# Kernel tuning notes

Measured on AMD Instinct MI355X. Metric: run time of the kernel, lower is better.

The kernel has to match this reference:

```python
import jax, jax.numpy as jnp
import numpy as np

B, S, H, F, V, MAX_OOV = 128, 512, 1024, 512, 50000, 50


def setup_inputs() -> dict:
    key = jax.random.key(0)
    ks = jax.random.split(key, 20)
    r = lambda i, shp, s=0.02: (jax.random.normal(ks[i], shp, jnp.float32) * s)
    return dict(
        input=jax.random.randint(ks[0], (B,), 0, V),
        hidden=jax.random.normal(ks[1], (1, B, H), jnp.float32) * 0.1,
        encoder_outputs=jax.random.normal(ks[2], (B, S, H), jnp.float32) * 0.1,
        x_padding_masks=jnp.ones((B, S), jnp.float32),
        len_oov=jax.random.randint(ks[3], (B,), 0, MAX_OOV),
        coverage_vector=jnp.zeros((B, S), jnp.float32),
        ref2tgt=jax.random.randint(ks[4], (B, S), 0, V + MAX_OOV),
        emb=r(5, (V, F)),
        W_ih=r(6, (3 * H, F)), W_hh=r(7, (3 * H, H)),
        b_ih=jnp.zeros(3 * H, jnp.float32), b_hh=jnp.zeros(3 * H, jnp.float32),
        e2v1_w=r(8, (F, H)), e2v1_b=jnp.zeros(F, jnp.float32),
        e2v2_w=r(9, (V, F)), e2v2_b=jnp.zeros(V, jnp.float32),
        fc_w=r(10, (H, 2 * H)), fc_b=jnp.zeros(H, jnp.float32),
        wgen_w=r(11, (1, 2 * H + F)), wgen_b=jnp.zeros(1, jnp.float32),
        att_Wh=r(12, (H, H)), att_Ws=r(13, (H, H)),
        att_wc=r(14, (H,)), att_b=jnp.zeros(H, jnp.float32), att_v=r(15, (H,)),
    )


def reference(input, hidden, encoder_outputs, x_padding_masks, len_oov,
              coverage_vector, ref2tgt, emb, W_ih, W_hh, b_ih, b_hh,
              e2v1_w, e2v1_b, e2v2_w, e2v2_b, fc_w, fc_b, wgen_w, wgen_b,
              att_Wh, att_Ws, att_wc, att_b, att_v):
    # embedding lookup (dropout is identity at inference)
    emb_x = emb[input]  # [B, F]

    # --- additive (Bahdanau) attention with coverage ---
    s = hidden[0]  # [B, H] (n_layers == 1)
    feat = jnp.tanh(
        jnp.einsum('bsh,kh->bsk', encoder_outputs, att_Wh)
        + (s @ att_Ws.T)[:, None, :]
        + coverage_vector[:, :, None] * att_wc
        + att_b)  # [B, S, H]
    e = jnp.einsum('bsh,h->bs', feat, att_v)  # [B, S]
    a = jax.nn.softmax(e, axis=1) * x_padding_masks
    a = a / (jnp.sum(a, axis=1, keepdims=True))  # [B, S] renormalized attn
    coverage_new = coverage_vector + a
    context = jnp.einsum('bs,bsh->bh', a, encoder_outputs)  # [B, H]
    h_att = jnp.concatenate([s, context], axis=-1) @ fc_w.T + fc_b  # [B, H]

    # --- single-step GRU (PyTorch gate order r, z, n) ---
    gi = emb_x @ W_ih.T + b_ih  # [B, 3H]
    gh = h_att @ W_hh.T + b_hh  # [B, 3H]
    i_r, i_z, i_n = jnp.split(gi, 3, axis=-1)
    h_r, h_z, h_n = jnp.split(gh, 3, axis=-1)
    r = jax.nn.sigmoid(i_r + h_r)
    z = jax.nn.sigmoid(i_z + h_z)
    n = jnp.tanh(i_n + r * h_n)
    h_new = (1.0 - z) * n + z * h_att  # [B, H]

    # --- vocab distribution ---
    out1 = h_new @ e2v1_w.T + e2v1_b  # [B, F]
    p_vocab = jax.nn.softmax(out1 @ e2v2_w.T + e2v2_b, axis=1)  # [B, V]

    # --- pointer-generator mixing ---
    x_gen = jnp.concatenate([context, h_new, emb_x], axis=-1)  # [B, 2H+F]
    p_gen = jax.nn.sigmoid(x_gen @ wgen_w.T + wgen_b)[:, 0]  # [B]
    p_gen = jnp.clip(p_gen, 0.001, 0.999)
    p_vocab_w = p_gen[:, None] * p_vocab  # [B, V]
    attn_w = (1.0 - p_gen)[:, None] * a  # [B, S]
    p_ext = jnp.concatenate([p_vocab_w, jnp.zeros((B, MAX_OOV), p_vocab_w.dtype)], axis=1)
    rows = jnp.arange(B)[:, None]
    final = p_ext.at[rows, ref2tgt].add(attn_w)  # scatter_add over extended vocab

    return final, h_new[None], coverage_new, a
```

## Files before the change

kernel.cpp:

```cpp
#include <hip/hip_runtime.h>
#include <math.h>

#define B_   128
#define S_   512
#define H_   1024
#define F_   512
#define V_   50000
#define OOV_ 50
#define EV_  (V_ + OOV_)

#define BM 128
#define BN 128
#define BK 64

typedef __attribute__((ext_vector_type(8))) __bf16 bf16x8;
typedef __attribute__((ext_vector_type(4))) __bf16 bf16x4;
typedef __attribute__((ext_vector_type(4))) float  f32x4;

__device__ __forceinline__ void gload_lds16(const void* g, void* lds) {
  __builtin_amdgcn_global_load_lds(
      (const __attribute__((address_space(1))) unsigned int*)g,
      (__attribute__((address_space(3))) unsigned int*)lds, 16, 0, 0);
}

__device__ __forceinline__ float fast_tanh(float x) {
  float v = fminf(fmaxf(x, -15.f), 15.f);
  float t = __expf(2.f * v);
  return 1.f - 2.f / (t + 1.f);
}

__global__ __launch_bounds__(256)
void cast_both_kernel(const float* __restrict__ enc, __bf16* __restrict__ enc_h,
                      const float* __restrict__ wh, __bf16* __restrict__ wh_h)
{
  const size_t n_enc = (size_t)B_ * S_ * H_;
  const size_t n_tot = n_enc + (size_t)H_ * H_;
  for (size_t i = ((size_t)blockIdx.x * 256 + threadIdx.x) * 8; i < n_tot;
       i += (size_t)gridDim.x * 256 * 8) {
    const float* in; __bf16* out; size_t j;
    if (i < n_enc) { in = enc; out = enc_h; j = i; }
    else           { in = wh;  out = wh_h;  j = i - n_enc; }
    float4 a = *(const float4*)(in + j);
    float4 b = *(const float4*)(in + j + 4);
    bf16x8 o;
    o[0] = (__bf16)a.x; o[1] = (__bf16)a.y; o[2] = (__bf16)a.z; o[3] = (__bf16)a.w;
    o[4] = (__bf16)b.x; o[5] = (__bf16)b.y; o[6] = (__bf16)b.z; o[7] = (__bf16)b.w;
    *(bf16x8*)(out + j) = o;
  }
}

__global__ __launch_bounds__(256)
void gemm_splitk(const float* __restrict__ A, const float* __restrict__ W,
                 float* __restrict__ partial, int N, int K, int KS)
{
  __shared__ float As[128 * 68];
  __shared__ float Ws[32 * 68];
  const int tid = threadIdx.x;
  const int n0 = blockIdx.x * 32;
  const int p  = blockIdx.y;
  const int tx = tid & 7, ty = tid >> 3;
  const int lr = tid >> 4, lc4 = (tid & 15) * 4;
  float acc[4][4] = {};
  const int kend = p * KS + KS;
  for (int k0 = p * KS; k0 < kend; k0 += 64) {
#pragma unroll
    for (int pp = 0; pp < 8; ++pp)
      *(float4*)(As + (pp * 16 + lr) * 68 + lc4) =
          *(const float4*)(A + (size_t)(pp * 16 + lr) * K + k0 + lc4);
#pragma unroll
    for (int pp = 0; pp < 2; ++pp)
      *(float4*)(Ws + (pp * 16 + lr) * 68 + lc4) =
          *(const float4*)(W + (size_t)(n0 + pp * 16 + lr) * K + k0 + lc4);
    __syncthreads();
#pragma unroll
    for (int kk = 0; kk < 16; ++kk) {
      float4 av[4], wv[4];
#pragma unroll
      for (int i = 0; i < 4; i++) av[i] = *(const float4*)(As + (ty * 4 + i) * 68 + kk * 4);
#pragma unroll
      for (int j = 0; j < 4; j++) wv[j] = *(const float4*)(Ws + (tx * 4 + j) * 68 + kk * 4);
#pragma unroll
      for (int i = 0; i < 4; i++)
#pragma unroll
        for (int j = 0; j < 4; j++) {
          acc[i][j] = fmaf(av[i].x, wv[j].x, acc[i][j]);
          acc[i][j] = fmaf(av[i].y, wv[j].y, acc[i][j]);
          acc[i][j] = fmaf(av[i].z, wv[j].z, acc[i][j]);
          acc[i][j] = fmaf(av[i].w, wv[j].w, acc[i][j]);
        }
    }
    __syncthreads();
  }
#pragma unroll
  for (int i = 0; i < 4; i++)
#pragma unroll
    for (int j = 0; j < 4; j++)
      partial[((size_t)p * 128 + ty * 4 + i) * N + n0 + tx * 4 + j] = acc[i][j];
}

__global__ __launch_bounds__(256)
void gemm_splitk_cat(const float* __restrict__ A1, const float* __restrict__ A2,
                     const float* __restrict__ W, float* __restrict__ partial,
                     int N, int K, int KS)
{
  __shared__ float As[128 * 68];
  __shared__ float Ws[32 * 68];
  const int tid = threadIdx.x;
  const int n0 = blockIdx.x * 32;
  const int p  = blockIdx.y;
  const int tx = tid & 7, ty = tid >> 3;
  const int lr = tid >> 4, lc4 = (tid & 15) * 4;
  const float* A = (p * KS < 1024) ? A1 : A2;
  const int kbase = (p * KS < 1024) ? 0 : 1024;
  float acc[4][4] = {};
  const int kend = p * KS + KS;
  for (int k0 = p * KS; k0 < kend; k0 += 64) {
#pragma unroll
    for (int pp = 0; pp < 8; ++pp)
      *(float4*)(As + (pp * 16 + lr) * 68 + lc4) =
          *(const float4*)(A + (size_t)(pp * 16 + lr) * 1024 + (k0 - kbase) + lc4);
#pragma unroll
    for (int pp = 0; pp < 2; ++pp)
      *(float4*)(Ws + (pp * 16 + lr) * 68 + lc4) =
          *(const float4*)(W + (size_t)(n0 + pp * 16 + lr) * K + k0 + lc4);
    __syncthreads();
#pragma unroll
    for (int kk = 0; kk < 16; ++kk) {
      float4 av[4], wv[4];
#pragma unroll
      for (int i = 0; i < 4; i++) av[i] = *(const float4*)(As + (ty * 4 + i) * 68 + kk * 4);
#pragma unroll
      for (int j = 0; j < 4; j++) wv[j] = *(const float4*)(Ws + (tx * 4 + j) * 68 + kk * 4);
#pragma unroll
      for (int i = 0; i < 4; i++)
#pragma unroll
        for (int j = 0; j < 4; j++) {
          acc[i][j] = fmaf(av[i].x, wv[j].x, acc[i][j]);
          acc[i][j] = fmaf(av[i].y, wv[j].y, acc[i][j]);
          acc[i][j] = fmaf(av[i].z, wv[j].z, acc[i][j]);
          acc[i][j] = fmaf(av[i].w, wv[j].w, acc[i][j]);
        }
    }
    __syncthreads();
  }
#pragma unroll
  for (int i = 0; i < 4; i++)
#pragma unroll
    for (int j = 0; j < 4; j++)
      partial[((size_t)p * 128 + ty * 4 + i) * N + n0 + tx * 4 + j] = acc[i][j];
}

__global__ __launch_bounds__(256)
void gemm_splitk_gather(const int* __restrict__ input, const float* __restrict__ emb,
                        const float* __restrict__ W, float* __restrict__ partial,
                        int N, int K, int KS)
{
  __shared__ float As[128 * 68];
  __shared__ float Ws[32 * 68];
  const int tid = threadIdx.x;
  const int n0 = blockIdx.x * 32;
  const int p  = blockIdx.y;
  const int tx = tid & 7, ty = tid >> 3;
  const int lr = tid >> 4, lc4 = (tid & 15) * 4;
  float acc[4][4] = {};
  const int kend = p * KS + KS;
  for (int k0 = p * KS; k0 < kend; k0 += 64) {
#pragma unroll
    for (int pp = 0; pp < 8; ++pp) {
      int row = input[pp * 16 + lr];
      *(float4*)(As + (pp * 16 + lr) * 68 + lc4) =
          *(const float4*)(emb + (size_t)row * K + k0 + lc4);
    }
#pragma unroll
    for (int pp = 0; pp < 2; ++pp)
      *(float4*)(Ws + (pp * 16 + lr) * 68 + lc4) =
          *(const float4*)(W + (size_t)(n0 + pp * 16 + lr) * K + k0 + lc4);
    __syncthreads();
#pragma unroll
    for (int kk = 0; kk < 16; ++kk) {
      float4 av[4], wv[4];
#pragma unroll
      for (int i = 0; i < 4; i++) av[i] = *(const float4*)(As + (ty * 4 + i) * 68 + kk * 4);
#pragma unroll
      for (int j = 0; j < 4; j++) wv[j] = *(const float4*)(Ws + (tx * 4 + j) * 68 + kk * 4);
#pragma unroll
      for (int i = 0; i < 4; i++)
#pragma unroll
        for (int j = 0; j < 4; j++) {
          acc[i][j] = fmaf(av[i].x, wv[j].x, acc[i][j]);
          acc[i][j] = fmaf(av[i].y, wv[j].y, acc[i][j]);
          acc[i][j] = fmaf(av[i].z, wv[j].z, acc[i][j]);
          acc[i][j] = fmaf(av[i].w, wv[j].w, acc[i][j]);
        }
    }
    __syncthreads();
  }
#pragma unroll
  for (int i = 0; i < 4; i++)
#pragma unroll
    for (int j = 0; j < 4; j++)
      partial[((size_t)p * 128 + ty * 4 + i) * N + n0 + tx * 4 + j] = acc[i][j];
}

__global__ __launch_bounds__(256)
void reduce_partial(const float* __restrict__ partial, const float* __restrict__ bias,
                    float* __restrict__ C, int N, int P)
{
  int idx = blockIdx.x * 256 + threadIdx.x;
  int n = idx % N;
  float s = bias ? bias[n] : 0.f;
  for (int p = 0; p < P; ++p) s += partial[(size_t)p * 128 * N + idx];
  C[idx] = s;
}

__global__ __launch_bounds__(256)
void reduce_partial_bf16(const float* __restrict__ partial, const float* __restrict__ bias,
                         __bf16* __restrict__ C, int N, int P)
{
  int idx = blockIdx.x * 256 + threadIdx.x;
  int n = idx % N;
  float s = bias ? bias[n] : 0.f;
  for (int p = 0; p < P; ++p) s += partial[(size_t)p * 128 * N + idx];
  C[idx] = (__bf16)s;
}

__global__ __launch_bounds__(256)
void feat_mfma_kernel(const __bf16* __restrict__ enc, const __bf16* __restrict__ Wh,
                      const float* __restrict__ pSWS, const float* __restrict__ cov,
                      const float* __restrict__ wcv, const float* __restrict__ ab,
                      const float* __restrict__ av_, float* __restrict__ e_part)
{
  __shared__ __attribute__((aligned(16))) __bf16 As[BM * BK];
  __shared__ __attribute__((aligned(16))) __bf16 Bs[BN * BK];
  __shared__ float red[BM][2];
  const int tid  = threadIdx.x;
  const int lane = tid & 63, wid = tid >> 6;
  const int wr = wid >> 1, wcc = wid & 1;
  const int bid = blockIdx.x;
  const int swz = (bid & 7) * 512 + (bid >> 3);
  const int bs0 = (swz >> 3) * BM;
  const int n0  = (swz & 7) * BN;
  const int b   = bs0 / S_;

  f32x4 acc[4][4];
#pragma unroll
  for (int i = 0; i < 4; i++)
#pragma unroll
    for (int j = 0; j < 4; j++) acc[i][j] = (f32x4){0.f, 0.f, 0.f, 0.f};

  for (int k0 = 0; k0 < H_; k0 += BK) {
#pragma unroll
    for (int p = 0; p < 4; ++p) {
      int off = p * 4096 + tid * 16;
      int r = off >> 7, cb = off & 127;
      int scb = cb ^ ((r & 7) << 4);
      gload_lds16(enc + (size_t)(bs0 + r) * H_ + k0 + (scb >> 1), (char*)As + off);
      gload_lds16(Wh  + (size_t)(n0 + r) * H_ + k0 + (scb >> 1), (char*)Bs + off);
    }
    __syncthreads();

    bf16x8 af[4][2], bfv[4][2];
#pragma unroll
    for (int m = 0; m < 4; ++m) {
      int row = wr * 64 + m * 16 + (lane & 15);
      int swzb = (row & 7) << 4;
#pragma unroll
      for (int kk = 0; kk < 2; ++kk) {
        int kb = kk * 64 + ((lane >> 4) << 4);
        af[m][kk] = *(const bf16x8*)((const char*)As + row * 128 + (kb ^ swzb));
      }
    }
#pragma unroll
    for (int n = 0; n < 4; ++n) {
      int row = wcc * 64 + n * 16 + (lane & 15);
      int swzb = (row & 7) << 4;
#pragma unroll
      for (int kk = 0; kk < 2; ++kk) {
        int kb = kk * 64 + ((lane >> 4) << 4);
        bfv[n][kk] = *(const bf16x8*)((const char*)Bs + row * 128 + (kb ^ swzb));
      }
    }
#pragma unroll
    for (int m = 0; m < 4; ++m)
#pragma unroll
      for (int n = 0; n < 4; ++n)
#pragma unroll
        for (int kk = 0; kk < 2; ++kk)
          acc[m][n] = __builtin_amdgcn_mfma_f32_16x16x32_bf16(af[m][kk], bfv[n][kk], acc[m][n], 0, 0, 0);
    __syncthreads();
  }

  float rowsum[4][4];
#pragma unroll
  for (int m = 0; m < 4; m++)
#pragma unroll
    for (int j = 0; j < 4; j++) rowsum[m][j] = 0.f;

#pragma unroll
  for (int n = 0; n < 4; ++n) {
    int col_g = n0 + wcc * 64 + n * 16 + (lane & 15);
    float sw = 0.f;
#pragma unroll
    for (int p = 0; p < 16; ++p) sw += pSWS[((size_t)p * 128 + b) * H_ + col_g];
    float wc_n = wcv[col_g], ab_n = ab[col_g], av_n = av_[col_g];
#pragma unroll
    for (int m = 0; m < 4; ++m) {
#pragma unroll
      for (int j = 0; j < 4; ++j) {
        int row_l = wr * 64 + m * 16 + ((lane >> 4) << 2) + j;
        float val = acc[m][n][j] + sw + cov[bs0 + row_l] * wc_n + ab_n;
        rowsum[m][j] += fast_tanh(val) * av_n;
      }
    }
  }
#pragma unroll
  for (int m = 0; m < 4; ++m)
#pragma unroll
    for (int j = 0; j < 4; ++j) {
      float v = rowsum[m][j];
      v += __shfl_xor(v, 1);
      v += __shfl_xor(v, 2);
      v += __shfl_xor(v, 4);
      v += __shfl_xor(v, 8);
      rowsum[m][j] = v;
    }
  if ((lane & 15) == 0) {
#pragma unroll
    for (int m = 0; m < 4; ++m)
#pragma unroll
      for (int j = 0; j < 4; ++j)
        red[wr * 64 + m * 16 + ((lane >> 4) << 2) + j][wcc] = rowsum[m][j];
  }
  __syncthreads();
  if (tid < BM)
    e_part[(size_t)(swz & 7) * (B_ * S_) + bs0 + tid] = red[tid][0] + red[tid][1];
}

__global__ __launch_bounds__(256)
void logits_mfma_kernel(const __bf16* __restrict__ A, const float* __restrict__ W,
                        const float* __restrict__ bias, float* __restrict__ out0)
{
  __shared__ __attribute__((aligned(16))) __bf16 As[BM * BK];
  __shared__ __attribute__((aligned(16))) __bf16 Bs[BN * BK];
  const int tid  = threadIdx.x;
  const int lane = tid & 63, wid = tid >> 6;
  const int wr = wid >> 1, wcc = wid & 1;
  const int n0 = blockIdx.x * BN;

  f32x4 acc[4][4];
#pragma unroll
  for (int i = 0; i < 4; i++)
#pragma unroll
    for (int j = 0; j < 4; j++) acc[i][j] = (f32x4){0.f, 0.f, 0.f, 0.f};

  for (int k0 = 0; k0 < F_; k0 += BK) {
#pragma unroll
    for (int p = 0; p < 4; ++p) {
      int off = p * 4096 + tid * 16;
      int r = off >> 7, cb = off & 127;
      int scb = cb ^ ((r & 7) << 4);
      gload_lds16(A + (size_t)r * F_ + k0 + (scb >> 1), (char*)As + off);
    }
#pragma unroll
    for (int p = 0; p < 8; ++p) {
      int idx = p * 1024 + tid * 4;
      int r = idx >> 6, c = idx & 63;
      int row_g = n0 + r; if (row_g >= V_) row_g = V_ - 1;
      float4 f = *(const float4*)(W + (size_t)row_g * F_ + k0 + c);
      union { __bf16 h[4]; uint2 u; } t;
      t.h[0] = (__bf16)f.x; t.h[1] = (__bf16)f.y; t.h[2] = (__bf16)f.z; t.h[3] = (__bf16)f.w;
      int cb = c * 2;
      *(uint2*)((char*)Bs + r * 128 + (cb ^ ((r & 7) << 4))) = t.u;
    }
    __syncthreads();

    bf16x8 af[4][2], bfv[4][2];
#pragma unroll
    for (int m = 0; m < 4; ++m) {
      int row = wr * 64 + m * 16 + (lane & 15);
      int swz = (row & 7) << 4;
#pragma unroll
      for (int kk = 0; kk < 2; ++kk) {
        int kb = kk * 64 + ((lane >> 4) << 4);
        af[m][kk] = *(const bf16x8*)((const char*)As + row * 128 + (kb ^ swz));
      }
    }
#pragma unroll
    for (int n = 0; n < 4; ++n) {
      int row = wcc * 64 + n * 16 + (lane & 15);
      int swz = (row & 7) << 4;
#pragma unroll
      for (int kk = 0; kk < 2; ++kk) {
        int kb = kk * 64 + ((lane >> 4) << 4);
        bfv[n][kk] = *(const bf16x8*)((const char*)Bs + row * 128 + (kb ^ swz));
      }
    }
#pragma unroll
    for (int m = 0; m < 4; ++m)
#pragma unroll
      for (int n = 0; n < 4; ++n)
#pragma unroll
        for (int kk = 0; kk < 2; ++kk)
          acc[m][n] = __builtin_amdgcn_mfma_f32_16x16x32_bf16(af[m][kk], bfv[n][kk], acc[m][n], 0, 0, 0);
    __syncthreads();
  }

#pragma unroll
  for (int m = 0; m < 4; ++m) {
#pragma unroll
    for (int n = 0; n < 4; ++n) {
      int col_g = n0 + wcc * 64 + n * 16 + (lane & 15);
      if (col_g >= V_) continue;
      float bv = bias[col_g];
#pragma unroll
      for (int j = 0; j < 4; ++j) {
        int row = wr * 64 + m * 16 + ((lane >> 4) << 2) + j;
        out0[(size_t)row * EV_ + col_g] = acc[m][n][j] + bv;
      }
    }
  }
}

__global__ __launch_bounds__(512)
void softmax_a_kernel(const float* __restrict__ e_part, const float* __restrict__ mask,
                      const float* __restrict__ cov, float* __restrict__ a_ws,
                      float* __restrict__ out_a, float* __restrict__ out_cov)
{
  const int b = blockIdx.x;
  const int s = threadIdx.x;
  __shared__ float red[512];
  float e = 0.f;
  for (int kt = 0; kt < 8; ++kt) e += e_part[(size_t)kt * (B_ * S_) + b * S_ + s];
  red[s] = e;
  __syncthreads();
  for (int st = 256; st > 0; st >>= 1) {
    if (s < st) red[s] = fmaxf(red[s], red[s + st]);
    __syncthreads();
  }
  float mx = red[0];
  __syncthreads();
  float ex = expf(e - mx) * mask[b * S_ + s];
  red[s] = ex;
  __syncthreads();
  for (int st = 256; st > 0; st >>= 1) {
    if (s < st) red[s] += red[s + st];
    __syncthreads();
  }
  float a = ex / red[0];
  a_ws[b * S_ + s] = a;
  out_a[b * S_ + s] = a;
  out_cov[b * S_ + s] = cov[b * S_ + s] + a;
}

__global__ __launch_bounds__(256)
void context_kernel(const float* __restrict__ a_ws, const __bf16* __restrict__ enc,
                    float* __restrict__ ctx)
{
  const int b = blockIdx.y, q = blockIdx.x;
  const int lane = threadIdx.x & 63, w = threadIdx.x >> 6;
  const int h0 = q * 256 + lane * 4;
  __shared__ float al[S_];
  __shared__ float part[4][256];
  for (int i = threadIdx.x; i < S_; i += 256) al[i] = a_ws[b * S_ + i];
  __syncthreads();
  float acc0 = 0.f, acc1 = 0.f, acc2 = 0.f, acc3 = 0.f;
  const __bf16* ep = enc + (size_t)b * S_ * H_ + h0;
#pragma unroll 4
  for (int s = w * 128; s < w * 128 + 128; ++s) {
    bf16x4 v = *(const bf16x4*)(ep + (size_t)s * H_);
    float a = al[s];
    acc0 = fmaf(a, (float)v[0], acc0);
    acc1 = fmaf(a, (float)v[1], acc1);
    acc2 = fmaf(a, (float)v[2], acc2);
    acc3 = fmaf(a, (float)v[3], acc3);
  }
  part[w][lane * 4 + 0] = acc0;
  part[w][lane * 4 + 1] = acc1;
  part[w][lane * 4 + 2] = acc2;
  part[w][lane * 4 + 3] = acc3;
  __syncthreads();
  if (threadIdx.x < 256) {
    int o = threadIdx.x;
    if (o < 256)
      ctx[b * H_ + q * 256 + o] = part[0][o] + part[1][o] + part[2][o] + part[3][o];
  }
}

__global__ __launch_bounds__(256)
void gru_kernel(const float* __restrict__ pgi, const float* __restrict__ pgh,
                const float* __restrict__ b_ih, const float* __restrict__ b_hh,
                const float* __restrict__ h_att, float* __restrict__ h_new_ws,
                float* __restrict__ out_h)
{
  int idx = blockIdx.x * 256 + threadIdx.x;
  int b = idx >> 10, h = idx & 1023;
  float ir = b_ih[h], iz = b_ih[H_ + h], in_ = b_ih[2 * H_ + h];
  float hr = b_hh[h], hz = b_hh[H_ + h], hn = b_hh[2 * H_ + h];
#pragma unroll
  for (int p = 0; p < 8; ++p) {
    const float* gp = pgi + (size_t)p * 128 * 3072 + (size_t)b * 3072;
    ir += gp[h]; iz += gp[H_ + h]; in_ += gp[2 * H_ + h];
    const float* hp = pgh + (size_t)p * 128 * 3072 + (size_t)b * 3072;
    hr += hp[h]; hz += hp[H_ + h]; hn += hp[2 * H_ + h];
  }
  float r = 1.f / (1.f + expf(-(ir + hr)));
  float z = 1.f / (1.f + expf(-(iz + hz)));
  float n = tanhf(in_ + r * hn);
  float ha = h_att[(size_t)b * H_ + h];
  float hv = (1.f - z) * n + z * ha;
  h_new_ws[idx] = hv;
  out_h[idx] = hv;
}

__global__ __launch_bounds__(256)
void pgen_kernel(const float* __restrict__ context, const float* __restrict__ h_new,
                 const int* __restrict__ input, const float* __restrict__ emb,
                 const float* __restrict__ wgen_w, const float* __restrict__ wgen_b,
                 float* __restrict__ pgen)
{
  int b = blockIdx.x;
  const float* erow = emb + (size_t)input[b] * F_;
  float acc = 0.f;
  for (int j = threadIdx.x; j < H_; j += 256) acc = fmaf(context[b * H_ + j], wgen_w[j], acc);
  for (int j = threadIdx.x; j < H_; j += 256) acc = fmaf(h_new[b * H_ + j], wgen_w[H_ + j], acc);
  for (int j = threadIdx.x; j < F_; j += 256) acc = fmaf(erow[j], wgen_w[2 * H_ + j], acc);
  __shared__ float red[256];
  red[threadIdx.x] = acc;
  __syncthreads();
  for (int st = 128; st > 0; st >>= 1) {
    if (threadIdx.x < st) red[threadIdx.x] += red[threadIdx.x + st];
    __syncthreads();
  }
  if (threadIdx.x == 0) {
    float p = 1.f / (1.f + expf(-(red[0] + wgen_b[0])));
    p = fminf(fmaxf(p, 0.001f), 0.999f);
    pgen[b] = p;
  }
}

__global__ __launch_bounds__(512)
void vstats_kernel(const float* __restrict__ logits, float* __restrict__ vmax,
                   float* __restrict__ vsum)
{
  int b = blockIdx.x;
  const float* row = logits + (size_t)b * EV_;
  __shared__ float red[512];
  float m = -1e30f;
  for (int v = threadIdx.x; v < V_; v += 512) m = fmaxf(m, row[v]);
  red[threadIdx.x] = m;
  __syncthreads();
  for (int st = 256; st > 0; st >>= 1) {
    if (threadIdx.x < st) red[threadIdx.x] = fmaxf(red[threadIdx.x], red[threadIdx.x + st]);
    __syncthreads();
  }
  m = red[0];
  __syncthreads();
  float ssum = 0.f;
  for (int v = threadIdx.x; v < V_; v += 512) ssum += expf(row[v] - m);
  red[threadIdx.x] = ssum;
  __syncthreads();
  for (int st = 256; st > 0; st >>= 1) {
    if (threadIdx.x < st) red[threadIdx.x] += red[threadIdx.x + st];
    __syncthreads();
  }
  if (threadIdx.x == 0) { vmax[b] = m; vsum[b] = red[0]; }
}

__global__ void final_kernel(float* __restrict__ out0, const float* __restrict__ vmax,
                             const float* __restrict__ vsum, const float* __restrict__ pgen)
{
  int b = blockIdx.y;
  int v = blockIdx.x * 256 + threadIdx.x;
  if (v >= EV_) return;
  float* row = out0 + (size_t)b * EV_;
  if (v < V_) row[v] = pgen[b] * expf(row[v] - vmax[b]) / vsum[b];
  else row[v] = 0.f;
}

__global__ void scatter_kernel(const int* __restrict__ ref2tgt, const float* __restrict__ a_ws,
                               const float* __restrict__ pgen, float* __restrict__ out0)
{
  int b = blockIdx.x;
  int s = threadIdx.x;
  float w = (1.f - pgen[b]) * a_ws[b * S_ + s];
  int t = ref2tgt[b * S_ + s];
  atomicAdd(&out0[(size_t)b * EV_ + t], w);
}

extern "C" void kernel_launch(void* const* d_in, const int* in_sizes, int n_in,
                              void* d_out, int out_size, void* d_ws, size_t ws_size,
                              hipStream_t stream)
{
  const int*   input   = (const int*)d_in[0];
  const float* hidden  = (const float*)d_in[1];
  const float* enc     = (const float*)d_in[2];
  const float* mask    = (const float*)d_in[3];
  const float* cov     = (const float*)d_in[5];
  const int*   ref2tgt = (const int*)d_in[6];
  const float* emb     = (const float*)d_in[7];
  const float* W_ih    = (const float*)d_in[8];
  const float* W_hh    = (const float*)d_in[9];
  const float* b_ih    = (const float*)d_in[10];
  const float* b_hh    = (const float*)d_in[11];
  const float* e2v1_w  = (const float*)d_in[12];
  const float* e2v1_b  = (const float*)d_in[13];
  const float* e2v2_w  = (const float*)d_in[14];
  const float* e2v2_b  = (const float*)d_in[15];
  const float* fc_w    = (const float*)d_in[16];
  const float* fc_b    = (const float*)d_in[17];
  const float* wgen_w  = (const float*)d_in[18];
  const float* wgen_b  = (const float*)d_in[19];
  const float* att_Wh  = (const float*)d_in[20];
  const float* att_Ws  = (const float*)d_in[21];
  const float* att_wc  = (const float*)d_in[22];
  const float* att_b   = (const float*)d_in[23];
  const float* att_v   = (const float*)d_in[24];

  char* w = (char*)d_ws;
  __bf16* enc_h  = (__bf16*)w;  w += (size_t)B_ * S_ * H_ * 2;
  __bf16* Wh_h   = (__bf16*)w;  w += (size_t)H_ * H_ * 2;
  __bf16* out1_h = (__bf16*)w;  w += (size_t)B_ * F_ * 2;
  float* e_part  = (float*)w;   w += (size_t)8 * B_ * S_ * 4;
  float* a_ws    = (float*)w;   w += (size_t)B_ * S_ * 4;
  float* context = (float*)w;   w += (size_t)B_ * H_ * 4;
  float* h_att   = (float*)w;   w += (size_t)B_ * H_ * 4;
  float* h_new   = (float*)w;   w += (size_t)B_ * H_ * 4;
  float* pgen    = (float*)w;   w += 128 * 4;
  float* vmax    = (float*)w;   w += 128 * 4;
  float* vsum    = (float*)w;   w += 128 * 4;
  float* pA      = (float*)w;   w += (size_t)16 * 128 * 1024 * 4;
  float* pB      = (float*)w;   w += (size_t)8 * 128 * 3072 * 4;
  float* pC      = (float*)w;   w += (size_t)8 * 128 * 3072 * 4;

  float* out0    = (float*)d_out;
  float* out_h   = out0 + (size_t)B_ * EV_;
  float* out_cov = out_h + (size_t)B_ * H_;
  float* out_a   = out_cov + (size_t)B_ * S_;

  cast_both_kernel<<<4096, 256, 0, stream>>>(enc, enc_h, att_Wh, Wh_h);
  gemm_splitk<<<dim3(32, 16), 256, 0, stream>>>(hidden, att_Ws, pA, H_, H_, 64);
  feat_mfma_kernel<<<dim3(4096), 256, 0, stream>>>(enc_h, Wh_h, pA, cov, att_wc, att_b, att_v, e_part);
  softmax_a_kernel<<<B_, 512, 0, stream>>>(e_part, mask, cov, a_ws, out_a, out_cov);
  context_kernel<<<dim3(4, B_), 256, 0, stream>>>(a_ws, enc_h, context);
  gemm_splitk_cat<<<dim3(32, 16), 256, 0, stream>>>(hidden, context, fc_w, pA, H_, 2 * H_, 128);
  reduce_partial<<<512, 256, 0, stream>>>(pA, fc_b, h_att, H_, 16);
  gemm_splitk_gather<<<dim3(96, 8), 256, 0, stream>>>(input, emb, W_ih, pB, 3 * H_, F_, 64);
  gemm_splitk<<<dim3(96, 8), 256, 0, stream>>>(h_att, W_hh, pC, 3 * H_, H_, 128);
  gru_kernel<<<(B_ * H_) / 256, 256, 0, stream>>>(pB, pC, b_ih, b_hh, h_att, h_new, out_h);
  gemm_splitk<<<dim3(16, 16), 256, 0, stream>>>(h_new, e2v1_w, pA, F_, H_, 64);
  reduce_partial_bf16<<<256, 256, 0, stream>>>(pA, e2v1_b, out1_h, F_, 16);
  logits_mfma_kernel<<<dim3((V_ + BN - 1) / BN), 256, 0, stream>>>(out1_h, e2v2_w, e2v2_b, out0);
  pgen_kernel<<<B_, 256, 0, stream>>>(context, h_new, input, emb, wgen_w, wgen_b, pgen);
  vstats_kernel<<<B_, 512, 0, stream>>>(out0, vmax, vsum);
  final_kernel<<<dim3((EV_ + 255) / 256, B_), 256, 0, stream>>>(out0, vmax, vsum, pgen);
  scatter_kernel<<<B_, 512, 0, stream>>>(ref2tgt, a_ws, pgen, out0);
}
```

Baseline: 524.8 us.

## Enlarge attention feature GEMM tile to 256x256 with double-buffered LDS

Replaces the 128x128 attention-feature MFMA kernel with a 512-thread 256x256 tile that double-buffers the K-loop, issuing the next stage's global-to-LDS loads before computing on the current buffer. The larger tile halves the number of N-slices, so each encoder row is reloaded fewer times, and softmax now sums 4 partials instead of 8. The split-K partials of s@Ws are reduced once in a separate kernel instead of being summed 16 times per column inside every feature block. In exchange, register and LDS pressure rise, which may limit occupancy.

Result: faster. 500.3 us (-4.7%).

```diff
diff --git a/kernel.cpp b/kernel.cpp
--- a/kernel.cpp
+++ b/kernel.cpp
@@ -12,6 +12,10 @@
 #define BM 128
 #define BN 128
 #define BK 64
+
+#define BM2 256
+#define BN2 256
+#define BK2 64
 
 typedef __attribute__((ext_vector_type(8))) __bf16 bf16x8;
 typedef __attribute__((ext_vector_type(4))) __bf16 bf16x4;
@@ -224,97 +228,106 @@
   C[idx] = (__bf16)s;
 }
 
-__global__ __launch_bounds__(256)
-void feat_mfma_kernel(const __bf16* __restrict__ enc, const __bf16* __restrict__ Wh,
-                      const float* __restrict__ pSWS, const float* __restrict__ cov,
-                      const float* __restrict__ wcv, const float* __restrict__ ab,
-                      const float* __restrict__ av_, float* __restrict__ e_part)
-{
-  __shared__ __attribute__((aligned(16))) __bf16 As[BM * BK];
-  __shared__ __attribute__((aligned(16))) __bf16 Bs[BN * BK];
-  __shared__ float red[BM][2];
+__global__ __launch_bounds__(512, 2)
+void feat_mfma256_kernel(const __bf16* __restrict__ enc, const __bf16* __restrict__ Wh,
+                         const float* __restrict__ sws, const float* __restrict__ cov,
+                         const float* __restrict__ wcv, const float* __restrict__ ab,
+                         const float* __restrict__ av_, float* __restrict__ e_part)
+{
+  __shared__ __attribute__((aligned(16))) __bf16 As[2][BM2 * BK2];
+  __shared__ __attribute__((aligned(16))) __bf16 Bs[2][BN2 * BK2];
   const int tid  = threadIdx.x;
   const int lane = tid & 63, wid = tid >> 6;
-  const int wr = wid >> 1, wcc = wid & 1;
+  const int wr = wid >> 2, wc = wid & 3;
   const int bid = blockIdx.x;
-  const int swz = (bid & 7) * 512 + (bid >> 3);
-  const int bs0 = (swz >> 3) * BM;
-  const int n0  = (swz & 7) * BN;
-  const int b   = bs0 / S_;
-
-  f32x4 acc[4][4];
-#pragma unroll
-  for (int i = 0; i < 4; i++)
+  const int swz = (bid & 7) * 128 + (bid >> 3);
+  const int mt = swz >> 2, nt = swz & 3;
+  const int bs0 = mt * BM2;
+  const int n0  = nt * BN2;
+  const int b   = bs0 >> 9;
+
+  f32x4 acc[8][4];
+#pragma unroll
+  for (int i = 0; i < 8; i++)
 #pragma unroll
     for (int j = 0; j < 4; j++) acc[i][j] = (f32x4){0.f, 0.f, 0.f, 0.f};
 
-  for (int k0 = 0; k0 < H_; k0 += BK) {
-#pragma unroll
-    for (int p = 0; p < 4; ++p) {
-      int off = p * 4096 + tid * 16;
-      int r = off >> 7, cb = off & 127;
-      int scb = cb ^ ((r & 7) << 4);
-      gload_lds16(enc + (size_t)(bs0 + r) * H_ + k0 + (scb >> 1), (char*)As + off);
-      gload_lds16(Wh  + (size_t)(n0 + r) * H_ + k0 + (scb >> 1), (char*)Bs + off);
-    }
-    __syncthreads();
-
-    bf16x8 af[4][2], bfv[4][2];
-#pragma unroll
-    for (int m = 0; m < 4; ++m) {
-      int row = wr * 64 + m * 16 + (lane & 15);
-      int swzb = (row & 7) << 4;
+#define STAGE2(c, k0)                                                          \
+  {                                                                            \
+    _Pragma("unroll")                                                          \
+    for (int p = 0; p < 4; ++p) {                                              \
+      int off = p * 8192 + tid * 16;                                           \
+      int r = off >> 7, cb = off & 127;                                        \
+      int scb = cb ^ ((r & 7) << 4);                                           \
+      gload_lds16(enc + (size_t)(bs0 + r) * H_ + (k0) + (scb >> 1),            \
+                  (char*)As[c] + off);                                         \
+      gload_lds16(Wh + (size_t)(n0 + r) * H_ + (k0) + (scb >> 1),              \
+                  (char*)Bs[c] + off);                                         \
+    }                                                                          \
+  }
+
+  STAGE2(0, 0)
+  __syncthreads();
+
+  int cur = 0;
+  for (int kt = 0; kt < 16; ++kt) {
+    if (kt < 15) STAGE2(cur ^ 1, (kt + 1) * BK2)
+
+    bf16x8 bfv[4][2];
+#pragma unroll
+    for (int n = 0; n < 4; ++n) {
+      int row = wc * 64 + n * 16 + (lane & 15);
+      int sw = (row & 7) << 4;
 #pragma unroll
       for (int kk = 0; kk < 2; ++kk) {
         int kb = kk * 64 + ((lane >> 4) << 4);
-        af[m][kk] = *(const bf16x8*)((const char*)As + row * 128 + (kb ^ swzb));
+        bfv[n][kk] = *(const bf16x8*)((const char*)Bs[cur] + row * 128 + (kb ^ sw));
       }
     }
 #pragma unroll
-    for (int n = 0; n < 4; ++n) {
-      int row = wcc * 64 + n * 16 + (lane & 15);
-      int swzb = (row & 7) << 4;
+    for (int m = 0; m < 8; ++m) {
+      int row = wr * 128 + m * 16 + (lane & 15);
+      int sw = (row & 7) << 4;
+      bf16x8 af[2];
 #pragma unroll
       for (int kk = 0; kk < 2; ++kk) {
         int kb = kk * 64 + ((lane >> 4) << 4);
-        bfv[n][kk] = *(const bf16x8*)((const char*)Bs + row * 128 + (kb ^ swzb));
+        af[kk] = *(const bf16x8*)((const char*)As[cur] + row * 128 + (kb ^ sw));
       }
-    }
-#pragma unroll
-    for (int m = 0; m < 4; ++m)
 #pragma unroll
       for (int n = 0; n < 4; ++n)
 #pragma unroll
         for (int kk = 0; kk < 2; ++kk)
-          acc[m][n] = __builtin_amdgcn_mfma_f32_16x16x32_bf16(af[m][kk], bfv[n][kk], acc[m][n], 0, 0, 0);
-    __syncthreads();
-  }
-
-  float rowsum[4][4];
-#pragma unroll
-  for (int m = 0; m < 4; m++)
+          acc[m][n] = __builtin_amdgcn_mfma_f32_16x16x32_bf16(af[kk], bfv[n][kk], acc[m][n], 0, 0, 0);
+    }
+    __syncthreads();
+    cur ^= 1;
+  }
+#undef STAGE2
+
+  float rowsum[8][4];
+#pragma unroll
+  for (int m = 0; m < 8; m++)
 #pragma unroll
     for (int j = 0; j < 4; j++) rowsum[m][j] = 0.f;
 
 #pragma unroll
   for (int n = 0; n < 4; ++n) {
-    int col_g = n0 + wcc * 64 + n * 16 + (lane & 15);
-    float sw = 0.f;
-#pragma unroll
-    for (int p = 0; p < 16; ++p) sw += pSWS[((size_t)p * 128 + b) * H_ + col_g];
+    int col_g = n0 + wc * 64 + n * 16 + (lane & 15);
+    float sw   = sws[(size_t)b * H_ + col_g];
     float wc_n = wcv[col_g], ab_n = ab[col_g], av_n = av_[col_g];
 #pragma unroll
-    for (int m = 0; m < 4; ++m) {
+    for (int m = 0; m < 8; ++m) {
 #pragma unroll
       for (int j = 0; j < 4; ++j) {
-        int row_l = wr * 64 + m * 16 + ((lane >> 4) << 2) + j;
+        int row_l = wr * 128 + m * 16 + ((lane >> 4) << 2) + j;
         float val = acc[m][n][j] + sw + cov[bs0 + row_l] * wc_n + ab_n;
         rowsum[m][j] += fast_tanh(val) * av_n;
       }
     }
   }
 #pragma unroll
-  for (int m = 0; m < 4; ++m)
+  for (int m = 0; m < 8; ++m)
 #pragma unroll
     for (int j = 0; j < 4; ++j) {
       float v = rowsum[m][j];
@@ -324,16 +337,18 @@
       v += __shfl_xor(v, 8);
       rowsum[m][j] = v;
     }
+  float (*red)[4] = (float(*)[4])As;
   if ((lane & 15) == 0) {
 #pragma unroll
-    for (int m = 0; m < 4; ++m)
+    for (int m = 0; m < 8; ++m)
 #pragma unroll
       for (int j = 0; j < 4; ++j)
-        red[wr * 64 + m * 16 + ((lane >> 4) << 2) + j][wcc] = rowsum[m][j];
-  }
-  __syncthreads();
-  if (tid < BM)
-    e_part[(size_t)(swz & 7) * (B_ * S_) + bs0 + tid] = red[tid][0] + red[tid][1];
+        red[wr * 128 + m * 16 + ((lane >> 4) << 2) + j][wc] = rowsum[m][j];
+  }
+  __syncthreads();
+  if (tid < BM2)
+    e_part[(size_t)nt * (B_ * S_) + bs0 + tid] =
+        red[tid][0] + red[tid][1] + red[tid][2] + red[tid][3];
 }
 
 __global__ __launch_bounds__(256)
@@ -430,7 +445,7 @@
   const int s = threadIdx.x;
   __shared__ float red[512];
   float e = 0.f;
-  for (int kt = 0; kt < 8; ++kt) e += e_part[(size_t)kt * (B_ * S_) + b * S_ + s];
+  for (int kt = 0; kt < 4; ++kt) e += e_part[(size_t)kt * (B_ * S_) + b * S_ + s];
   red[s] = e;
   __syncthreads();
   for (int st = 256; st > 0; st >>= 1) {
@@ -481,8 +496,7 @@
   __syncthreads();
   if (threadIdx.x < 256) {
     int o = threadIdx.x;
-    if (o < 256)
-      ctx[b * H_ + q * 256 + o] = part[0][o] + part[1][o] + part[2][o] + part[3][o];
+    ctx[b * H_ + q * 256 + o] = part[0][o] + part[1][o] + part[2][o] + part[3][o];
   }
 }
 
@@ -620,7 +634,8 @@
   __bf16* enc_h  = (__bf16*)w;  w += (size_t)B_ * S_ * H_ * 2;
   __bf16* Wh_h   = (__bf16*)w;  w += (size_t)H_ * H_ * 2;
   __bf16* out1_h = (__bf16*)w;  w += (size_t)B_ * F_ * 2;
-  float* e_part  = (float*)w;   w += (size_t)8 * B_ * S_ * 4;
+  float* sws     = (float*)w;   w += (size_t)B_ * H_ * 4;
+  float* e_part  = (float*)w;   w += (size_t)4 * B_ * S_ * 4;
   float* a_ws    = (float*)w;   w += (size_t)B_ * S_ * 4;
   float* context = (float*)w;   w += (size_t)B_ * H_ * 4;
   float* h_att   = (float*)w;   w += (size_t)B_ * H_ * 4;
@@ -639,7 +654,8 @@
 
   cast_both_kernel<<<4096, 256, 0, stream>>>(enc, enc_h, att_Wh, Wh_h);
   gemm_splitk<<<dim3(32, 16), 256, 0, stream>>>(hidden, att_Ws, pA, H_, H_, 64);
-  feat_mfma_kernel<<<dim3(4096), 256, 0, stream>>>(enc_h, Wh_h, pA, cov, att_wc, att_b, att_v, e_part);
+  reduce_partial<<<512, 256, 0, stream>>>(pA, nullptr, sws, H_, 16);
+  feat_mfma256_kernel<<<dim3(1024), 512, 0, stream>>>(enc_h, Wh_h, sws, cov, att_wc, att_b, att_v, e_part);
   softmax_a_kernel<<<B_, 512, 0, stream>>>(e_part, mask, cov, a_ws, out_a, out_cov);
   context_kernel<<<dim3(4, B_), 256, 0, stream>>>(a_ws, enc_h, context);
   gemm_splitk_cat<<<dim3(32, 16), 256, 0, stream>>>(hidden, context, fc_w, pA, H_, 2 * H_, 128);
```

## Double-buffer LDS in attention feature GEMM and merge small tail kernels

Applied to the files above, without the earlier changes.

The attention feature MFMA kernel now double-buffers its A/B LDS tiles, issuing the next tile's global-to-LDS loads while computing on the current one. It also precomputes load and LDS-read offsets and raises the occupancy hint via launch_bounds(256,2). The 16-way split-K sum for s@Ws moves out of the per-tile epilogue into a separate reduce kernel, and the pgen and vocab-stats kernels merge into a single launch. Doubling LDS use may cap occupancy, and the extra reduce launch adds a little overhead.

After: 511.7 us. 1.03x faster.

```diff
diff --git a/kernel.cpp b/kernel.cpp
--- a/kernel.cpp
+++ b/kernel.cpp
@@ -224,14 +224,14 @@
   C[idx] = (__bf16)s;
 }
 
-__global__ __launch_bounds__(256)
+__global__ __launch_bounds__(256, 2)
 void feat_mfma_kernel(const __bf16* __restrict__ enc, const __bf16* __restrict__ Wh,
-                      const float* __restrict__ pSWS, const float* __restrict__ cov,
+                      const float* __restrict__ sws, const float* __restrict__ cov,
                       const float* __restrict__ wcv, const float* __restrict__ ab,
                       const float* __restrict__ av_, float* __restrict__ e_part)
 {
-  __shared__ __attribute__((aligned(16))) __bf16 As[BM * BK];
-  __shared__ __attribute__((aligned(16))) __bf16 Bs[BN * BK];
+  __shared__ __attribute__((aligned(16))) __bf16 As[2][BM * BK];
+  __shared__ __attribute__((aligned(16))) __bf16 Bs[2][BN * BK];
   __shared__ float red[BM][2];
   const int tid  = threadIdx.x;
   const int lane = tid & 63, wid = tid >> 6;
@@ -240,7 +240,33 @@
   const int swz = (bid & 7) * 512 + (bid >> 3);
   const int bs0 = (swz >> 3) * BM;
   const int n0  = (swz & 7) * BN;
-  const int b   = bs0 / S_;
+  const int b   = bs0 >> 9;
+
+  const int scb = ((tid & 7) * 16) ^ (((tid >> 3) & 7) << 4);
+  const __bf16* aPtr[2];
+  const __bf16* aP[4]; const __bf16* bP[4]; int ldsO[4];
+#pragma unroll
+  for (int p = 0; p < 4; ++p) {
+    int r = p * 32 + (tid >> 3);
+    ldsO[p] = p * 4096 + tid * 16;
+    aP[p] = enc + (size_t)(bs0 + r) * H_ + (scb >> 1);
+    bP[p] = Wh  + (size_t)(n0  + r) * H_ + (scb >> 1);
+  }
+  (void)aPtr;
+
+  const int swf = (lane & 7) << 4;
+  int aO[4][2], bO[4][2];
+#pragma unroll
+  for (int m = 0; m < 4; ++m) {
+    int rowa = wr * 64 + m * 16 + (lane & 15);
+    int rowb = wcc * 64 + m * 16 + (lane & 15);
+#pragma unroll
+    for (int kk = 0; kk < 2; ++kk) {
+      int kb = kk * 64 + ((lane >> 4) << 4);
+      aO[m][kk] = rowa * 128 + (kb ^ swf);
+      bO[m][kk] = rowb * 128 + (kb ^ swf);
+    }
+  }
 
   f32x4 acc[4][4];
 #pragma unroll
@@ -248,47 +274,50 @@
 #pragma unroll
     for (int j = 0; j < 4; j++) acc[i][j] = (f32x4){0.f, 0.f, 0.f, 0.f};
 
-  for (int k0 = 0; k0 < H_; k0 += BK) {
-#pragma unroll
-    for (int p = 0; p < 4; ++p) {
-      int off = p * 4096 + tid * 16;
-      int r = off >> 7, cb = off & 127;
-      int scb = cb ^ ((r & 7) << 4);
-      gload_lds16(enc + (size_t)(bs0 + r) * H_ + k0 + (scb >> 1), (char*)As + off);
-      gload_lds16(Wh  + (size_t)(n0 + r) * H_ + k0 + (scb >> 1), (char*)Bs + off);
-    }
-    __syncthreads();
-
-    bf16x8 af[4][2], bfv[4][2];
-#pragma unroll
-    for (int m = 0; m < 4; ++m) {
-      int row = wr * 64 + m * 16 + (lane & 15);
-      int swzb = (row & 7) << 4;
-#pragma unroll
-      for (int kk = 0; kk < 2; ++kk) {
-        int kb = kk * 64 + ((lane >> 4) << 4);
-        af[m][kk] = *(const bf16x8*)((const char*)As + row * 128 + (kb ^ swzb));
-      }
-    }
-#pragma unroll
-    for (int n = 0; n < 4; ++n) {
-      int row = wcc * 64 + n * 16 + (lane & 15);
-      int swzb = (row & 7) << 4;
-#pragma unroll
-      for (int kk = 0; kk < 2; ++kk) {
-        int kb = kk * 64 + ((lane >> 4) << 4);
-        bfv[n][kk] = *(const bf16x8*)((const char*)Bs + row * 128 + (kb ^ swzb));
-      }
-    }
-#pragma unroll
-    for (int m = 0; m < 4; ++m)
-#pragma unroll
-      for (int n = 0; n < 4; ++n)
-#pragma unroll
-        for (int kk = 0; kk < 2; ++kk)
-          acc[m][n] = __builtin_amdgcn_mfma_f32_16x16x32_bf16(af[m][kk], bfv[n][kk], acc[m][n], 0, 0, 0);
-    __syncthreads();
-  }
+#define STAGE(c, ofs)                                                          \
+  {                                                                            \
+    _Pragma("unroll")                                                          \
+    for (int p = 0; p < 4; ++p) {                                              \
+      gload_lds16(aP[p] + (ofs), (char*)As[c] + ldsO[p]);                      \
+      gload_lds16(bP[p] + (ofs), (char*)Bs[c] + ldsO[p]);                      \
+    }                                                                          \
+  }
+
+#define COMPUTE(c)                                                             \
+  {                                                                            \
+    bf16x8 bfv[4][2];                                                          \
+    _Pragma("unroll")                                                          \
+    for (int n = 0; n < 4; ++n)                                                \
+      _Pragma("unroll")                                                        \
+      for (int kk = 0; kk < 2; ++kk)                                           \
+        bfv[n][kk] = *(const bf16x8*)((const char*)Bs[c] + bO[n][kk]);         \
+    _Pragma("unroll")                                                          \
+    for (int m = 0; m < 4; ++m) {                                              \
+      bf16x8 a0 = *(const bf16x8*)((const char*)As[c] + aO[m][0]);             \
+      bf16x8 a1 = *(const bf16x8*)((const char*)As[c] + aO[m][1]);             \
+      _Pragma("unroll")                                                        \
+      for (int n = 0; n < 4; ++n) {                                            \
+        acc[m][n] = __builtin_amdgcn_mfma_f32_16x16x32_bf16(a0, bfv[n][0], acc[m][n], 0, 0, 0); \
+        acc[m][n] = __builtin_amdgcn_mfma_f32_16x16x32_bf16(a1, bfv[n][1], acc[m][n], 0, 0, 0); \
+      }                                                                        \
+    }                                                                          \
+  }
+
+  STAGE(0, 0)
+  __syncthreads();
+
+  for (int t2 = 0; t2 < 8; ++t2) {
+    STAGE(1, 64)
+    COMPUTE(0)
+    __syncthreads();
+    if (t2 < 7) STAGE(0, 128)
+    COMPUTE(1)
+    __syncthreads();
+#pragma unroll
+    for (int p = 0; p < 4; ++p) { aP[p] += 128; bP[p] += 128; }
+  }
+#undef STAGE
+#undef COMPUTE
 
   float rowsum[4][4];
 #pragma unroll
@@ -299,9 +328,7 @@
 #pragma unroll
   for (int n = 0; n < 4; ++n) {
     int col_g = n0 + wcc * 64 + n * 16 + (lane & 15);
-    float sw = 0.f;
-#pragma unroll
-    for (int p = 0; p < 16; ++p) sw += pSWS[((size_t)p * 128 + b) * H_ + col_g];
+    float sw   = sws[(size_t)b * H_ + col_g];
     float wc_n = wcv[col_g], ab_n = ab[col_g], av_n = av_[col_g];
 #pragma unroll
     for (int m = 0; m < 4; ++m) {
@@ -481,8 +508,7 @@
   __syncthreads();
   if (threadIdx.x < 256) {
     int o = threadIdx.x;
-    if (o < 256)
-      ctx[b * H_ + q * 256 + o] = part[0][o] + part[1][o] + part[2][o] + part[3][o];
+    ctx[b * H_ + q * 256 + o] = part[0][o] + part[1][o] + part[2][o] + part[3][o];
   }
 }
 
@@ -512,58 +538,55 @@
   out_h[idx] = hv;
 }
 
-__global__ __launch_bounds__(256)
-void pgen_kernel(const float* __restrict__ context, const float* __restrict__ h_new,
-                 const int* __restrict__ input, const float* __restrict__ emb,
-                 const float* __restrict__ wgen_w, const float* __restrict__ wgen_b,
-                 float* __restrict__ pgen)
-{
-  int b = blockIdx.x;
-  const float* erow = emb + (size_t)input[b] * F_;
-  float acc = 0.f;
-  for (int j = threadIdx.x; j < H_; j += 256) acc = fmaf(context[b * H_ + j], wgen_w[j], acc);
-  for (int j = threadIdx.x; j < H_; j += 256) acc = fmaf(h_new[b * H_ + j], wgen_w[H_ + j], acc);
-  for (int j = threadIdx.x; j < F_; j += 256) acc = fmaf(erow[j], wgen_w[2 * H_ + j], acc);
-  __shared__ float red[256];
-  red[threadIdx.x] = acc;
-  __syncthreads();
-  for (int st = 128; st > 0; st >>= 1) {
-    if (threadIdx.x < st) red[threadIdx.x] += red[threadIdx.x + st];
-    __syncthreads();
-  }
-  if (threadIdx.x == 0) {
-    float p = 1.f / (1.f + expf(-(red[0] + wgen_b[0])));
-    p = fminf(fmaxf(p, 0.001f), 0.999f);
-    pgen[b] = p;
-  }
-}
-
 __global__ __launch_bounds__(512)
-void vstats_kernel(const float* __restrict__ logits, float* __restrict__ vmax,
-                   float* __restrict__ vsum)
-{
-  int b = blockIdx.x;
-  const float* row = logits + (size_t)b * EV_;
+void stats_pgen_kernel(const float* __restrict__ logits, float* __restrict__ vmax,
+                       float* __restrict__ vsum, const float* __restrict__ context,
+                       const float* __restrict__ h_new, const int* __restrict__ input,
+                       const float* __restrict__ emb, const float* __restrict__ wgen_w,
+                       const float* __restrict__ wgen_b, float* __restrict__ pgen)
+{
   __shared__ float red[512];
-  float m = -1e30f;
-  for (int v = threadIdx.x; v < V_; v += 512) m = fmaxf(m, row[v]);
-  red[threadIdx.x] = m;
-  __syncthreads();
-  for (int st = 256; st > 0; st >>= 1) {
-    if (threadIdx.x < st) red[threadIdx.x] = fmaxf(red[threadIdx.x], red[threadIdx.x + st]);
-    __syncthreads();
-  }
-  m = red[0];
-  __syncthreads();
-  float ssum = 0.f;
-  for (int v = threadIdx.x; v < V_; v += 512) ssum += expf(row[v] - m);
-  red[threadIdx.x] = ssum;
-  __syncthreads();
-  for (int st = 256; st > 0; st >>= 1) {
-    if (threadIdx.x < st) red[threadIdx.x] += red[threadIdx.x + st];
-    __syncthreads();
-  }
-  if (threadIdx.x == 0) { vmax[b] = m; vsum[b] = red[0]; }
+  if (blockIdx.x < B_) {
+    int b = blockIdx.x;
+    const float* row = logits + (size_t)b * EV_;
+    float m = -1e30f;
+    for (int v = threadIdx.x; v < V_; v += 512) m = fmaxf(m, row[v]);
+    red[threadIdx.x] = m;
+    __syncthreads();
+    for (int st = 256; st > 0; st >>= 1) {
+      if (threadIdx.x < st) red[threadIdx.x] = fmaxf(red[threadIdx.x], red[threadIdx.x + st]);
+      __syncthreads();
+    }
+    m = red[0];
+    __syncthreads();
+    float ssum = 0.f;
+    for (int v = threadIdx.x; v < V_; v += 512) ssum += expf(row[v] - m);
+    red[threadIdx.x] = ssum;
+    __syncthreads();
+    for (int st = 256; st > 0; st >>= 1) {
+      if (threadIdx.x < st) red[threadIdx.x] += red[threadIdx.x + st];
+      __syncthreads();
+    }
+    if (threadIdx.x == 0) { vmax[b] = m; vsum[b] = red[0]; }
+  } else {
+    int b = blockIdx.x - B_;
+    const float* erow = emb + (size_t)input[b] * F_;
+    float acc = 0.f;
+    for (int j = threadIdx.x; j < H_; j += 512) acc = fmaf(context[b * H_ + j], wgen_w[j], acc);
+    for (int j = threadIdx.x; j < H_; j += 512) acc = fmaf(h_new[b * H_ + j], wgen_w[H_ + j], acc);
+    for (int j = threadIdx.x; j < F_; j += 512) acc = fmaf(erow[j], wgen_w[2 * H_ + j], acc);
+    red[threadIdx.x] = acc;
+    __syncthreads();
+    for (int st = 256; st > 0; st >>= 1) {
+      if (threadIdx.x < st) red[threadIdx.x] += red[threadIdx.x + st];
+      __syncthreads();
+    }
+    if (threadIdx.x == 0) {
+      float p = 1.f / (1.f + expf(-(red[0] + wgen_b[0])));
+      p = fminf(fmaxf(p, 0.001f), 0.999f);
+      pgen[b] = p;
+    }
+  }
 }
 
 __global__ void final_kernel(float* __restrict__ out0, const float* __restrict__ vmax,
@@ -620,6 +643,7 @@
   __bf16* enc_h  = (__bf16*)w;  w += (size_t)B_ * S_ * H_ * 2;
   __bf16* Wh_h   = (__bf16*)w;  w += (size_t)H_ * H_ * 2;
   __bf16* out1_h = (__bf16*)w;  w += (size_t)B_ * F_ * 2;
+  float* sws     = (float*)w;   w += (size_t)B_ * H_ * 4;
   float* e_part  = (float*)w;   w += (size_t)8 * B_ * S_ * 4;
   float* a_ws    = (float*)w;   w += (size_t)B_ * S_ * 4;
   float* context = (float*)w;   w += (size_t)B_ * H_ * 4;
@@ -639,7 +663,8 @@
 
   cast_both_kernel<<<4096, 256, 0, stream>>>(enc, enc_h, att_Wh, Wh_h);
   gemm_splitk<<<dim3(32, 16), 256, 0, stream>>>(hidden, att_Ws, pA, H_, H_, 64);
-  feat_mfma_kernel<<<dim3(4096), 256, 0, stream>>>(enc_h, Wh_h, pA, cov, att_wc, att_b, att_v, e_part);
+  reduce_partial<<<512, 256, 0, stream>>>(pA, nullptr, sws, H_, 16);
+  feat_mfma_kernel<<<dim3(4096), 256, 0, stream>>>(enc_h, Wh_h, sws, cov, att_wc, att_b, att_v, e_part);
   softmax_a_kernel<<<B_, 512, 0, stream>>>(e_part, mask, cov, a_ws, out_a, out_cov);
   context_kernel<<<dim3(4, B_), 256, 0, stream>>>(a_ws, enc_h, context);
   gemm_splitk_cat<<<dim3(32, 16), 256, 0, stream>>>(hidden, context, fc_w, pA, H_, 2 * H_, 128);
@@ -650,8 +675,8 @@
   gemm_splitk<<<dim3(16, 16), 256, 0, stream>>>(h_new, e2v1_w, pA, F_, H_, 64);
   reduce_partial_bf16<<<256, 256, 0, stream>>>(pA, e2v1_b, out1_h, F_, 16);
   logits_mfma_kernel<<<dim3((V_ + BN - 1) / BN), 256, 0, stream>>>(out1_h, e2v2_w, e2v2_b, out0);
-  pgen_kernel<<<B_, 256, 0, stream>>>(context, h_new, input, emb, wgen_w, wgen_b, pgen);
-  vstats_kernel<<<B_, 512, 0, stream>>>(out0, vmax, vsum);
+  stats_pgen_kernel<<<2 * B_, 512, 0, stream>>>(out0, vmax, vsum, context, h_new, input, emb,
+                                                wgen_w, wgen_b, pgen);
   final_kernel<<<dim3((EV_ + 255) / 256, B_), 256, 0, stream>>>(out0, vmax, vsum, pgen);
   scatter_kernel<<<B_, 512, 0, stream>>>(ref2tgt, a_ws, pgen, out0);
 }
```
